# Kernel tuning notes

Measured on AMD Instinct MI355X. Metric: run time of the kernel, lower is better.

Reference implementation:

```python
import jax, jax.numpy as jnp
import numpy as np

N, F_IN, H, O = 4096, 512, 4, 256
ALPHA = 0.2  # leaky-relu negative slope
NEG = -9e15  # mask value for non-edges (matches DAEGC)


def setup_inputs() -> dict:
    key = jax.random.key(0)
    ks = jax.random.split(key, 9)
    x = jax.random.normal(ks[0], (N, F_IN), jnp.float32)
    adj = (jax.random.uniform(ks[1], (N, N)) < 0.01).astype(jnp.float32)
    adj = jnp.maximum(adj, jnp.eye(N, dtype=jnp.float32))
    M = jax.random.uniform(ks[2], (N, N), dtype=jnp.float32)  # proximity matrix
    s0 = 1.0 / np.sqrt(F_IN)
    s1 = 1.0 / np.sqrt(H * O)
    W0 = jax.random.normal(ks[3], (H, F_IN, O), jnp.float32) * s0
    a_self0 = jax.random.normal(ks[4], (H, O), jnp.float32) * 0.1
    a_neigh0 = jax.random.normal(ks[5], (H, O), jnp.float32) * 0.1
    W1 = jax.random.normal(ks[6], (H, H * O, O), jnp.float32) * s1
    a_self1 = jax.random.normal(ks[7], (H, O), jnp.float32) * 0.1
    a_neigh1 = jax.random.normal(ks[8], (H, O), jnp.float32) * 0.1
    return dict(x=x, adj=adj, M=M, W0=W0, a_self0=a_self0, a_neigh0=a_neigh0,
                W1=W1, a_self1=a_self1, a_neigh1=a_neigh1)


def gat_layer(x, adj, M, W, a_s, a_n, concat):
    # x: [N, F_in], W: [H, F_in, O]
    h = jnp.einsum('nf,hfo->hno', x, W)                      # [H, N, O]
    e = (jnp.einsum('hno,ho->hn', h, a_s)[:, :, None]
         + jnp.einsum('hno,ho->hn', h, a_n)[:, None, :])     # [H, N, N]
    e = jax.nn.leaky_relu(e * M[None], ALPHA)
    e = jnp.where(adj[None] > 0, e, NEG)
    attn = jax.nn.softmax(e, axis=-1)                        # masked neighbor softmax
    out = jnp.einsum('hnm,hmo->hno', attn, h)                # [H, N, O]
    if concat:
        return jax.nn.elu(out.transpose(1, 0, 2).reshape(x.shape[0], -1))  # [N, H*O]
    return out.mean(axis=0)                                  # [N, O]


def reference(x, adj, M, W0, a_self0, a_neigh0, W1, a_self1, a_neigh1):
    h = gat_layer(x, adj, M, W0, a_self0, a_neigh0, True)
    h = gat_layer(h, adj, M, W1, a_self1, a_neigh1, False)
    # F.normalize(h, p=2, dim=1) with eps=1e-12
    z = h / jnp.maximum(jnp.linalg.norm(h, axis=1, keepdims=True), 1e-12)
    A_pred = jax.nn.sigmoid(z @ z.T)                          # dot-product decode [N, N]
    return (A_pred, z)
```

## Files before the change

### kernel.cpp

```cpp
#include <hip/hip_runtime.h>
#include <hip/hip_bf16.h>
#include <math.h>

#define N_NODES 4096
#define F_IN0   512
#define HEADS   4
#define O_DIM   256
#define HO      1024
#define LRELU_A 0.2f
#define MAXE    192

typedef __bf16 bf16_t;
typedef bf16_t bf16x8 __attribute__((ext_vector_type(8)));
typedef float f32x4 __attribute__((ext_vector_type(4)));

__device__ __forceinline__ unsigned short f2b(float f) {
    __hip_bfloat16 t = __float2bfloat16(f);
    return __builtin_bit_cast(unsigned short, t);
}
__device__ __forceinline__ float b2f(unsigned short u) {
    unsigned int v = ((unsigned int)u) << 16;
    return __builtin_bit_cast(float, v);
}

#define GLOAD_LDS(g, l) \
    __builtin_amdgcn_global_load_lds((const __attribute__((address_space(1))) unsigned int*)(g), \
                                     (__attribute__((address_space(3))) unsigned int*)(l), 16, 0, 0)

__global__ __launch_bounds__(256) void f2bf_k(const float* __restrict__ src,
                                              unsigned short* __restrict__ dst, int n4) {
    int i = blockIdx.x * blockDim.x + threadIdx.x;
    if (i < n4) {
        float4 v = ((const float4*)src)[i];
        ushort4 o;
        o.x = f2b(v.x); o.y = f2b(v.y); o.z = f2b(v.z); o.w = f2b(v.w);
        ((ushort4*)dst)[i] = o;
    }
}

__global__ __launch_bounds__(256) void transpose_bf16(const float* __restrict__ W,
                                                      unsigned short* __restrict__ Wt,
                                                      int K, int O) {
    __shared__ float t[32][33];
    const float* Wh = W + (size_t)blockIdx.z * K * O;
    unsigned short* Wth = Wt + (size_t)blockIdx.z * K * O;
    const int k0 = blockIdx.x * 32, o0 = blockIdx.y * 32;
    const int tx = threadIdx.x, ty = threadIdx.y;
    for (int r = ty; r < 32; r += 8) t[r][tx] = Wh[(size_t)(k0 + r) * O + o0 + tx];
    __syncthreads();
    for (int r = ty; r < 32; r += 8)
        Wth[(size_t)(o0 + r) * K + k0 + tx] = f2b(t[tx][r]);
}

__global__ __launch_bounds__(256) void edges_k(const float* __restrict__ adj,
                                               const float* __restrict__ Mm,
                                               int* __restrict__ ecnt,
                                               int* __restrict__ eidx,
                                               float* __restrict__ eMv) {
    const int n = blockIdx.x;
    const int tid = threadIdx.x;
    __shared__ int cnt;
    if (tid == 0) cnt = 0;
    __syncthreads();
    const float* adjr = adj + (size_t)n * N_NODES;
    const float* Mr   = Mm  + (size_t)n * N_NODES;
    for (int m0 = tid * 4; m0 < N_NODES; m0 += 1024) {
        const float4 a4 = *(const float4*)&adjr[m0];
        const float av[4] = {a4.x, a4.y, a4.z, a4.w};
#pragma unroll
        for (int q = 0; q < 4; ++q) {
            if (av[q] > 0.f) {
                int m = m0 + q;
                int k = atomicAdd(&cnt, 1);
                eidx[(size_t)n * MAXE + k] = m;
                eMv[(size_t)n * MAXE + k]  = Mr[m];
            }
        }
    }
    __syncthreads();
    if (tid == 0) ecnt[n] = cnt;
}

__global__ __launch_bounds__(256) void mfma_nt(const bf16_t* __restrict__ A,
                                               const bf16_t* __restrict__ B,
                                               unsigned short* __restrict__ Cv,
                                               int K, int ldc,
                                               unsigned long long bStride,
                                               unsigned long long cStride) {
    B += blockIdx.z * bStride;
    const size_t zoff = (size_t)blockIdx.z * cStride;
    __shared__ bf16_t sA[128 * 32];
    __shared__ bf16_t sB[128 * 32];
    const int tid  = threadIdx.x;
    const int lane = tid & 63;
    const int wave = tid >> 6;
    const int wr = (wave >> 1) * 64;
    const int wc = (wave & 1) * 64;
    const int rowBase = blockIdx.x * 128;
    const int colBase = blockIdx.y * 128;
    const int l15  = lane & 15;
    const int quad = lane >> 4;

    const int sm = tid & 127;
    const int sc = tid >> 7;
    const bf16_t* aRow = A + (size_t)(rowBase + sm) * K + sc * 8;
    const bf16_t* bRow = B + (size_t)(colBase + sm) * K + sc * 8;
    bf16_t* sA0 = &sA[(tid & ~63) * 8];
    bf16_t* sA1 = &sA[(256 + (tid & ~63)) * 8];
    bf16_t* sB0 = &sB[(tid & ~63) * 8];
    bf16_t* sB1 = &sB[(256 + (tid & ~63)) * 8];

    f32x4 acc[4][4] = {};

    for (int k0 = 0; k0 < K; k0 += 32) {
        GLOAD_LDS(aRow + k0,      sA0);
        GLOAD_LDS(aRow + k0 + 16, sA1);
        GLOAD_LDS(bRow + k0,      sB0);
        GLOAD_LDS(bRow + k0 + 16, sB1);
        __syncthreads();
        bf16x8 af[4], bfr[4];
#pragma unroll
        for (int i = 0; i < 4; ++i) {
            af[i]  = *(bf16x8*)&sA[(quad * 128 + wr + i * 16 + l15) * 8];
            bfr[i] = *(bf16x8*)&sB[(quad * 128 + wc + i * 16 + l15) * 8];
        }
#pragma unroll
        for (int i = 0; i < 4; ++i)
#pragma unroll
            for (int j = 0; j < 4; ++j)
                acc[i][j] = __builtin_amdgcn_mfma_f32_16x16x32_bf16(af[i], bfr[j], acc[i][j], 0, 0, 0);
        __syncthreads();
    }

    const int orow = rowBase + wr + quad * 4;
    const int ocol = colBase + wc + l15;
#pragma unroll
    for (int i = 0; i < 4; ++i)
#pragma unroll
        for (int j = 0; j < 4; ++j)
#pragma unroll
            for (int r = 0; r < 4; ++r)
                Cv[zoff + (size_t)(orow + i * 16 + r) * ldc + ocol + j * 16] = f2b(acc[i][j][r]);
}

__global__ __launch_bounds__(256) void decode_k(const bf16_t* __restrict__ Z,
                                                float* __restrict__ out) {
    const int tid  = threadIdx.x;
    const int lane = tid & 63;
    const int wave = tid >> 6;
    const int rowBase = blockIdx.x * 128 + (wave >> 1) * 64;
    const int colBase = blockIdx.y * 128 + (wave & 1) * 64;
    const int l15  = lane & 15;
    const int quad = lane >> 4;
    const bf16_t* aBase = Z + (size_t)(rowBase + l15) * O_DIM + quad * 8;
    const bf16_t* bBase = Z + (size_t)(colBase + l15) * O_DIM + quad * 8;

    f32x4 acc[4][4] = {};
#pragma unroll
    for (int kc = 0; kc < 8; ++kc) {
        bf16x8 a[4], b[4];
#pragma unroll
        for (int i = 0; i < 4; ++i) {
            a[i] = *(const bf16x8*)(aBase + (size_t)i * 16 * O_DIM + kc * 32);
            b[i] = *(const bf16x8*)(bBase + (size_t)i * 16 * O_DIM + kc * 32);
        }
#pragma unroll
        for (int i = 0; i < 4; ++i)
#pragma unroll
            for (int j = 0; j < 4; ++j)
                acc[i][j] = __builtin_amdgcn_mfma_f32_16x16x32_bf16(a[i], b[j], acc[i][j], 0, 0, 0);
    }

    const int orow = rowBase + quad * 4;
    const int ocol = colBase + l15;
#pragma unroll
    for (int i = 0; i < 4; ++i)
#pragma unroll
        for (int j = 0; j < 4; ++j)
#pragma unroll
            for (int r = 0; r < 4; ++r) {
                float v = acc[i][j][r];
                out[(size_t)(orow + i * 16 + r) * N_NODES + ocol + j * 16] =
                    1.f / (1.f + expf(-v));
            }
}

__global__ __launch_bounds__(256) void scores_k(const unsigned short* __restrict__ hb,
                                                const float* __restrict__ a_s,
                                                const float* __restrict__ a_n,
                                                float* __restrict__ s_self4,
                                                float* __restrict__ s_neigh4) {
    const int n = blockIdx.x;
    const int head = threadIdx.x >> 6;
    const int lane = threadIdx.x & 63;
    const ushort4 hv = *(const ushort4*)&hb[(size_t)n * HO + head * O_DIM + lane * 4];
    const float4 av = *(const float4*)&a_s[head * O_DIM + lane * 4];
    const float4 nv = *(const float4*)&a_n[head * O_DIM + lane * 4];
    float h0 = b2f(hv.x), h1 = b2f(hv.y), h2 = b2f(hv.z), h3 = b2f(hv.w);
    float ps = h0 * av.x + h1 * av.y + h2 * av.z + h3 * av.w;
    float pn = h0 * nv.x + h1 * nv.y + h2 * nv.z + h3 * nv.w;
    for (int off = 32; off; off >>= 1) {
        ps += __shfl_down(ps, off, 64);
        pn += __shfl_down(pn, off, 64);
    }
    if (lane == 0) {
        s_self4[n * HEADS + head]  = ps;
        s_neigh4[n * HEADS + head] = pn;
    }
}

__global__ __launch_bounds__(256) void attn_k(const unsigned short* __restrict__ hb,
                                              const int* __restrict__ ecnt,
                                              const int* __restrict__ eidx,
                                              const float* __restrict__ eMv,
                                              const float* __restrict__ s_self4,
                                              const float* __restrict__ s_neigh4,
                                              unsigned short* __restrict__ out0,
                                              float* __restrict__ out1, int layer) {
    const int n = blockIdx.x;
    const int tid = threadIdx.x;
    __shared__ int midx[MAXE];
    __shared__ float ev[MAXE][HEADS];
    __shared__ float isum[HEADS];
    __shared__ float red[HO];
    const int c = ecnt[n];
    if (tid < c) {
        const int m = eidx[(size_t)n * MAXE + tid];
        const float Mv = eMv[(size_t)n * MAXE + tid];
        midx[tid] = m;
        const float4 ss = *(const float4*)&s_self4[n * HEADS];
        const float4 sn = *(const float4*)&s_neigh4[m * HEADS];
        float e0 = (ss.x + sn.x) * Mv, e1 = (ss.y + sn.y) * Mv;
        float e2 = (ss.z + sn.z) * Mv, e3 = (ss.w + sn.w) * Mv;
        ev[tid][0] = e0 > 0.f ? e0 : LRELU_A * e0;
        ev[tid][1] = e1 > 0.f ? e1 : LRELU_A * e1;
        ev[tid][2] = e2 > 0.f ? e2 : LRELU_A * e2;
        ev[tid][3] = e3 > 0.f ? e3 : LRELU_A * e3;
    }
    __syncthreads();
    if (tid < HEADS) {
        float mx = -1e30f;
        for (int k = 0; k < c; ++k) mx = fmaxf(mx, ev[k][tid]);
        float s = 0.f;
        for (int k = 0; k < c; ++k) {
            float p = expf(ev[k][tid] - mx);
            ev[k][tid] = p;
            s += p;
        }
        isum[tid] = 1.f / s;
    }
    __syncthreads();
    for (int i = tid; i < c * HEADS; i += 256) {
        int k = i >> 2, h = i & 3;
        ev[k][h] *= isum[h];
    }
    __syncthreads();
    const int head = tid >> 6;
    float a0 = 0.f, a1 = 0.f, a2 = 0.f, a3 = 0.f;
#pragma unroll 4
    for (int k = 0; k < c; ++k) {
        const int m = midx[k];
        const float w = ev[k][head];
        const ushort4 hv = *(const ushort4*)&hb[(size_t)m * HO + tid * 4];
        a0 += w * b2f(hv.x); a1 += w * b2f(hv.y);
        a2 += w * b2f(hv.z); a3 += w * b2f(hv.w);
    }
    if (layer == 0) {
        a0 = a0 > 0.f ? a0 : expm1f(a0);
        a1 = a1 > 0.f ? a1 : expm1f(a1);
        a2 = a2 > 0.f ? a2 : expm1f(a2);
        a3 = a3 > 0.f ? a3 : expm1f(a3);
        ushort4 o;
        o.x = f2b(a0); o.y = f2b(a1); o.z = f2b(a2); o.w = f2b(a3);
        *(ushort4*)&out0[(size_t)n * HO + tid * 4] = o;
    } else {
        red[tid * 4 + 0] = a0; red[tid * 4 + 1] = a1;
        red[tid * 4 + 2] = a2; red[tid * 4 + 3] = a3;
        __syncthreads();
        const int o = tid;
        out1[(size_t)n * O_DIM + o] =
            0.25f * (red[o] + red[O_DIM + o] + red[2 * O_DIM + o] + red[3 * O_DIM + o]);
    }
}

__global__ __launch_bounds__(256) void norm_k(float* __restrict__ z,
                                              unsigned short* __restrict__ zb) {
    const int n = blockIdx.x;
    const int tid = threadIdx.x;
    float v = z[(size_t)n * O_DIM + tid];
    float p = v * v;
    for (int off = 32; off; off >>= 1) p += __shfl_down(p, off, 64);
    __shared__ float wsum[4];
    if ((tid & 63) == 0) wsum[tid >> 6] = p;
    __syncthreads();
    float ssq = wsum[0] + wsum[1] + wsum[2] + wsum[3];
    float denom = fmaxf(sqrtf(ssq), 1e-12f);
    float zn = v / denom;
    z[(size_t)n * O_DIM + tid] = zn;
    zb[(size_t)n * O_DIM + tid] = f2b(zn);
}

extern "C" void kernel_launch(void* const* d_in, const int* in_sizes, int n_in,
                              void* d_out, int out_size, void* d_ws, size_t ws_size,
                              hipStream_t stream) {
    const float* x   = (const float*)d_in[0];
    const float* adj = (const float*)d_in[1];
    const float* Mm  = (const float*)d_in[2];
    const float* W0  = (const float*)d_in[3];
    const float* as0 = (const float*)d_in[4];
    const float* an0 = (const float*)d_in[5];
    const float* W1  = (const float*)d_in[6];
    const float* as1 = (const float*)d_in[7];
    const float* an1 = (const float*)d_in[8];
    float* out = (float*)d_out;

    unsigned short* hb    = (unsigned short*)d_ws;
    unsigned short* hin1b = hb + (size_t)N_NODES * HO;
    unsigned short* xb    = hin1b + (size_t)N_NODES * HO;
    unsigned short* wt0   = xb + (size_t)N_NODES * F_IN0;
    unsigned short* wt1   = wt0 + HEADS * O_DIM * F_IN0;
    unsigned short* zb    = wt1 + HEADS * O_DIM * HO;
    float* s_self4  = (float*)(zb + (size_t)N_NODES * O_DIM);
    float* s_neigh4 = s_self4 + N_NODES * HEADS;
    int*   eidx = (int*)(s_neigh4 + N_NODES * HEADS);
    float* eMv  = (float*)(eidx + (size_t)N_NODES * MAXE);
    int*   ecnt = (int*)(eMv + (size_t)N_NODES * MAXE);
    float* zbuf = out + (size_t)N_NODES * N_NODES;

    f2bf_k<<<2048, 256, 0, stream>>>(x, xb, 524288);
    transpose_bf16<<<dim3(16, 8, 4), dim3(32, 8), 0, stream>>>(W0, wt0, F_IN0, O_DIM);
    transpose_bf16<<<dim3(32, 8, 4), dim3(32, 8), 0, stream>>>(W1, wt1, HO, O_DIM);
    edges_k<<<N_NODES, 256, 0, stream>>>(adj, Mm, ecnt, eidx, eMv);

    mfma_nt<<<dim3(32, 2, 4), 256, 0, stream>>>((const bf16_t*)xb, (const bf16_t*)wt0, hb,
                                                F_IN0, HO,
                                                (unsigned long long)O_DIM * F_IN0,
                                                (unsigned long long)O_DIM);
    scores_k<<<N_NODES, 256, 0, stream>>>(hb, as0, an0, s_self4, s_neigh4);
    attn_k<<<N_NODES, 256, 0, stream>>>(hb, ecnt, eidx, eMv, s_self4, s_neigh4, hin1b, nullptr, 0);

    mfma_nt<<<dim3(32, 2, 4), 256, 0, stream>>>((const bf16_t*)hin1b, (const bf16_t*)wt1, hb,
                                                HO, HO,
                                                (unsigned long long)O_DIM * HO,
                                                (unsigned long long)O_DIM);
    scores_k<<<N_NODES, 256, 0, stream>>>(hb, as1, an1, s_self4, s_neigh4);
    attn_k<<<N_NODES, 256, 0, stream>>>(hb, ecnt, eidx, eMv, s_self4, s_neigh4, nullptr, zbuf, 1);

    norm_k<<<N_NODES, 256, 0, stream>>>(zbuf, zb);
    decode_k<<<dim3(32, 32), 256, 0, stream>>>((const bf16_t*)zb, out);
}
```

Baseline: 365.8 us.

## Merge prep kernels, parallelize softmax per wave, use fast exp/sigmoid intrinsics

Four preprocessing kernels (x cast, two weight transposes, edge extraction) are merged into one launch that dispatches on block index, which removes launch gaps. The attention softmax now runs across a full wave per head with shuffle reductions instead of four serial threads. The aggregation loop splits edges into two halves with wider 8-element loads and combines the halves in shared memory. Sigmoid, exp and ELU switch to exp2/rcp hardware intrinsics, which are slightly less precise.

```diff
diff --git a/kernel.cpp b/kernel.cpp
--- a/kernel.cpp
+++ b/kernel.cpp
@@ -9,10 +9,12 @@
 #define HO      1024
 #define LRELU_A 0.2f
 #define MAXE    192
+#define LOG2E   1.44269504088896f
 
 typedef __bf16 bf16_t;
 typedef bf16_t bf16x8 __attribute__((ext_vector_type(8)));
 typedef float f32x4 __attribute__((ext_vector_type(4)));
+typedef unsigned short u16x8 __attribute__((ext_vector_type(8)));
 
 __device__ __forceinline__ unsigned short f2b(float f) {
     __hip_bfloat16 t = __float2bfloat16(f);
@@ -22,63 +24,80 @@
     unsigned int v = ((unsigned int)u) << 16;
     return __builtin_bit_cast(float, v);
 }
+__device__ __forceinline__ float fexp(float x) {
+    return __builtin_amdgcn_exp2f(x * LOG2E);
+}
+__device__ __forceinline__ float fsigmoid(float x) {
+    return __builtin_amdgcn_rcpf(1.f + __builtin_amdgcn_exp2f(-x * LOG2E));
+}
 
 #define GLOAD_LDS(g, l) \
     __builtin_amdgcn_global_load_lds((const __attribute__((address_space(1))) unsigned int*)(g), \
                                      (__attribute__((address_space(3))) unsigned int*)(l), 16, 0, 0)
 
-__global__ __launch_bounds__(256) void f2bf_k(const float* __restrict__ src,
-                                              unsigned short* __restrict__ dst, int n4) {
-    int i = blockIdx.x * blockDim.x + threadIdx.x;
-    if (i < n4) {
-        float4 v = ((const float4*)src)[i];
+__device__ __forceinline__ void transpose_tile(const float* __restrict__ W,
+                                               unsigned short* __restrict__ Wt,
+                                               int K, int O, int kt, int ot, int h,
+                                               float (*t)[33], int tid) {
+    const float* Wh = W + (size_t)h * K * O;
+    unsigned short* Wth = Wt + (size_t)h * K * O;
+    const int k0 = kt * 32, o0 = ot * 32;
+    const int tx = tid & 31, ty = tid >> 5;
+    for (int r = ty; r < 32; r += 8) t[r][tx] = Wh[(size_t)(k0 + r) * O + o0 + tx];
+    __syncthreads();
+    for (int r = ty; r < 32; r += 8)
+        Wth[(size_t)(o0 + r) * K + k0 + tx] = f2b(t[tx][r]);
+}
+
+__global__ __launch_bounds__(256) void prep_k(const float* __restrict__ x,
+                                              const float* __restrict__ W0,
+                                              const float* __restrict__ W1,
+                                              const float* __restrict__ adj,
+                                              const float* __restrict__ Mm,
+                                              unsigned short* __restrict__ xb,
+                                              unsigned short* __restrict__ wt0,
+                                              unsigned short* __restrict__ wt1,
+                                              int* __restrict__ ecnt,
+                                              int* __restrict__ eidx,
+                                              float* __restrict__ eMv) {
+    __shared__ float t[32][33];
+    __shared__ int cnt;
+    const int b = blockIdx.x;
+    const int tid = threadIdx.x;
+    if (b < 2048) {
+        int i = b * 256 + tid;
+        float4 v = ((const float4*)x)[i];
         ushort4 o;
         o.x = f2b(v.x); o.y = f2b(v.y); o.z = f2b(v.z); o.w = f2b(v.w);
-        ((ushort4*)dst)[i] = o;
-    }
-}
-
-__global__ __launch_bounds__(256) void transpose_bf16(const float* __restrict__ W,
-                                                      unsigned short* __restrict__ Wt,
-                                                      int K, int O) {
-    __shared__ float t[32][33];
-    const float* Wh = W + (size_t)blockIdx.z * K * O;
-    unsigned short* Wth = Wt + (size_t)blockIdx.z * K * O;
-    const int k0 = blockIdx.x * 32, o0 = blockIdx.y * 32;
-    const int tx = threadIdx.x, ty = threadIdx.y;
-    for (int r = ty; r < 32; r += 8) t[r][tx] = Wh[(size_t)(k0 + r) * O + o0 + tx];
-    __syncthreads();
-    for (int r = ty; r < 32; r += 8)
-        Wth[(size_t)(o0 + r) * K + k0 + tx] = f2b(t[tx][r]);
-}
-
-__global__ __launch_bounds__(256) void edges_k(const float* __restrict__ adj,
-                                               const float* __restrict__ Mm,
-                                               int* __restrict__ ecnt,
-                                               int* __restrict__ eidx,
-                                               float* __restrict__ eMv) {
-    const int n = blockIdx.x;
-    const int tid = threadIdx.x;
-    __shared__ int cnt;
-    if (tid == 0) cnt = 0;
-    __syncthreads();
-    const float* adjr = adj + (size_t)n * N_NODES;
-    const float* Mr   = Mm  + (size_t)n * N_NODES;
-    for (int m0 = tid * 4; m0 < N_NODES; m0 += 1024) {
-        const float4 a4 = *(const float4*)&adjr[m0];
-        const float av[4] = {a4.x, a4.y, a4.z, a4.w};
-#pragma unroll
-        for (int q = 0; q < 4; ++q) {
-            if (av[q] > 0.f) {
-                int m = m0 + q;
-                int k = atomicAdd(&cnt, 1);
-                eidx[(size_t)n * MAXE + k] = m;
-                eMv[(size_t)n * MAXE + k]  = Mr[m];
+        ((ushort4*)xb)[i] = o;
+    } else if (b < 2560) {
+        int b2 = b - 2048;
+        transpose_tile(W0, wt0, F_IN0, O_DIM, (b2 & 15), ((b2 >> 4) & 7), b2 >> 7, t, tid);
+    } else if (b < 3584) {
+        int b2 = b - 2560;
+        transpose_tile(W1, wt1, HO, O_DIM, (b2 & 31), ((b2 >> 5) & 7), b2 >> 8, t, tid);
+    } else {
+        const int n = b - 3584;
+        if (tid == 0) cnt = 0;
+        __syncthreads();
+        const float* adjr = adj + (size_t)n * N_NODES;
+        const float* Mr   = Mm  + (size_t)n * N_NODES;
+        for (int m0 = tid * 4; m0 < N_NODES; m0 += 1024) {
+            const float4 a4 = *(const float4*)&adjr[m0];
+            const float av[4] = {a4.x, a4.y, a4.z, a4.w};
+#pragma unroll
+            for (int q = 0; q < 4; ++q) {
+                if (av[q] > 0.f) {
+                    int m = m0 + q;
+                    int k = atomicAdd(&cnt, 1);
+                    eidx[(size_t)n * MAXE + k] = m;
+                    eMv[(size_t)n * MAXE + k]  = Mr[m];
+                }
             }
         }
-    }
-    __syncthreads();
-    if (tid == 0) ecnt[n] = cnt;
+        __syncthreads();
+        if (tid == 0) ecnt[n] = cnt;
+    }
 }
 
 __global__ __launch_bounds__(256) void mfma_nt(const bf16_t* __restrict__ A,
@@ -178,11 +197,9 @@
 #pragma unroll
         for (int j = 0; j < 4; ++j)
 #pragma unroll
-            for (int r = 0; r < 4; ++r) {
-                float v = acc[i][j][r];
+            for (int r = 0; r < 4; ++r)
                 out[(size_t)(orow + i * 16 + r) * N_NODES + ocol + j * 16] =
-                    1.f / (1.f + expf(-v));
-            }
+                    fsigmoid(acc[i][j][r]);
 }
 
 __global__ __launch_bounds__(256) void scores_k(const unsigned short* __restrict__ hb,
@@ -221,9 +238,9 @@
     const int tid = threadIdx.x;
     __shared__ int midx[MAXE];
     __shared__ float ev[MAXE][HEADS];
-    __shared__ float isum[HEADS];
-    __shared__ float red[HO];
+    __shared__ float red2[2][HO];
     const int c = ecnt[n];
+
     if (tid < c) {
         const int m = eidx[(size_t)n * MAXE + tid];
         const float Mv = eMv[(size_t)n * MAXE + tid];
@@ -238,48 +255,59 @@
         ev[tid][3] = e3 > 0.f ? e3 : LRELU_A * e3;
     }
     __syncthreads();
-    if (tid < HEADS) {
+
+    {
+        const int w = tid >> 6, lane = tid & 63;
         float mx = -1e30f;
-        for (int k = 0; k < c; ++k) mx = fmaxf(mx, ev[k][tid]);
+        for (int k = lane; k < c; k += 64) mx = fmaxf(mx, ev[k][w]);
+        for (int off = 32; off; off >>= 1) mx = fmaxf(mx, __shfl_xor(mx, off, 64));
         float s = 0.f;
-        for (int k = 0; k < c; ++k) {
-            float p = expf(ev[k][tid] - mx);
-            ev[k][tid] = p;
+        for (int k = lane; k < c; k += 64) {
+            float p = fexp(ev[k][w] - mx);
+            ev[k][w] = p;
             s += p;
         }
-        isum[tid] = 1.f / s;
-    }
-    __syncthreads();
-    for (int i = tid; i < c * HEADS; i += 256) {
-        int k = i >> 2, h = i & 3;
-        ev[k][h] *= isum[h];
-    }
-    __syncthreads();
-    const int head = tid >> 6;
-    float a0 = 0.f, a1 = 0.f, a2 = 0.f, a3 = 0.f;
-#pragma unroll 4
-    for (int k = 0; k < c; ++k) {
+        for (int off = 32; off; off >>= 1) s += __shfl_xor(s, off, 64);
+        float inv = __builtin_amdgcn_rcpf(s);
+        for (int k = lane; k < c; k += 64) ev[k][w] *= inv;
+    }
+    __syncthreads();
+
+    const int half = tid >> 7;
+    const int t    = tid & 127;
+    const int hh   = t >> 5;
+    float acc[8] = {};
+#pragma unroll 2
+    for (int k = half; k < c; k += 2) {
         const int m = midx[k];
-        const float w = ev[k][head];
-        const ushort4 hv = *(const ushort4*)&hb[(size_t)m * HO + tid * 4];
-        a0 += w * b2f(hv.x); a1 += w * b2f(hv.y);
-        a2 += w * b2f(hv.z); a3 += w * b2f(hv.w);
-    }
+        const float w = ev[k][hh];
+        const u16x8 hv = *(const u16x8*)&hb[(size_t)m * HO + t * 8];
+#pragma unroll
+        for (int j = 0; j < 8; ++j) acc[j] += w * b2f(hv[j]);
+    }
+#pragma unroll
+    for (int j = 0; j < 8; ++j) red2[half][t * 8 + j] = acc[j];
+    __syncthreads();
+
     if (layer == 0) {
-        a0 = a0 > 0.f ? a0 : expm1f(a0);
-        a1 = a1 > 0.f ? a1 : expm1f(a1);
-        a2 = a2 > 0.f ? a2 : expm1f(a2);
-        a3 = a3 > 0.f ? a3 : expm1f(a3);
-        ushort4 o;
-        o.x = f2b(a0); o.y = f2b(a1); o.z = f2b(a2); o.w = f2b(a3);
-        *(ushort4*)&out0[(size_t)n * HO + tid * 4] = o;
+        const int o = tid * 4;
+        ushort4 ov;
+        float v0 = red2[0][o + 0] + red2[1][o + 0];
+        float v1 = red2[0][o + 1] + red2[1][o + 1];
+        float v2 = red2[0][o + 2] + red2[1][o + 2];
+        float v3 = red2[0][o + 3] + red2[1][o + 3];
+        ov.x = f2b(v0 > 0.f ? v0 : fexp(v0) - 1.f);
+        ov.y = f2b(v1 > 0.f ? v1 : fexp(v1) - 1.f);
+        ov.z = f2b(v2 > 0.f ? v2 : fexp(v2) - 1.f);
+        ov.w = f2b(v3 > 0.f ? v3 : fexp(v3) - 1.f);
+        *(ushort4*)&out0[(size_t)n * HO + o] = ov;
     } else {
-        red[tid * 4 + 0] = a0; red[tid * 4 + 1] = a1;
-        red[tid * 4 + 2] = a2; red[tid * 4 + 3] = a3;
-        __syncthreads();
         const int o = tid;
-        out1[(size_t)n * O_DIM + o] =
-            0.25f * (red[o] + red[O_DIM + o] + red[2 * O_DIM + o] + red[3 * O_DIM + o]);
+        float v = 0.f;
+#pragma unroll
+        for (int h = 0; h < HEADS; ++h)
+            v += red2[0][h * O_DIM + o] + red2[1][h * O_DIM + o];
+        out1[(size_t)n * O_DIM + o] = 0.25f * v;
     }
 }
 
@@ -327,10 +355,7 @@
     int*   ecnt = (int*)(eMv + (size_t)N_NODES * MAXE);
     float* zbuf = out + (size_t)N_NODES * N_NODES;
 
-    f2bf_k<<<2048, 256, 0, stream>>>(x, xb, 524288);
-    transpose_bf16<<<dim3(16, 8, 4), dim3(32, 8), 0, stream>>>(W0, wt0, F_IN0, O_DIM);
-    transpose_bf16<<<dim3(32, 8, 4), dim3(32, 8), 0, stream>>>(W1, wt1, HO, O_DIM);
-    edges_k<<<N_NODES, 256, 0, stream>>>(adj, Mm, ecnt, eidx, eMv);
+    prep_k<<<7680, 256, 0, stream>>>(x, W0, W1, adj, Mm, xb, wt0, wt1, ecnt, eidx, eMv);
 
     mfma_nt<<<dim3(32, 2, 4), 256, 0, stream>>>((const bf16_t*)xb, (const bf16_t*)wt0, hb,
                                                 F_IN0, HO,
```

Result: faster. 337.5 us (-7.7%).
